# Kernel optimization log

Hardware: AMD Instinct MI355X
Metric: run time of the kernel (lower is better)

Reference implementation:

```python
import jax, jax.numpy as jnp
import numpy as np

D = 512
H = 4
HD = D // H
FF = 4 * D
B = 512
T = 128
EMA_K = 128
LOC_K = 4
DECAY = 0.9
STEP = 0.5 / np.sqrt(128 / 32)  # 0.25
EPS = 1e-5


def layernorm(x, g, b):
    mu = jnp.mean(x, axis=-1, keepdims=True)
    var = jnp.mean(jnp.square(x - mu), axis=-1, keepdims=True)
    return (x - mu) * jax.lax.rsqrt(var + EPS) * g + b


def dwconv_causal(x, w):
    # x: (B,T,D), w: (D,K); torch Conv1d(groups=D, padding=K-1) sliced to [:T]
    K = w.shape[1]
    xt = jnp.transpose(x, (0, 2, 1))  # (B,D,T)
    y = jax.lax.conv_general_dilated(
        xt, w[:, None, :], window_strides=(1,), padding=[(K - 1, 0)],
        feature_group_count=x.shape[-1], dimension_numbers=('NCT', 'OIT', 'NCT'))
    return jnp.transpose(y, (0, 2, 1))


def rope(qk, cos, sin):
    # qk: (B,H,T,HD)
    x1, x2 = jnp.split(qk, 2, axis=-1)
    rot = jnp.concatenate([-x2, x1], axis=-1)
    return qk * cos + rot * sin


def setup_inputs() -> dict:
    key = jax.random.key(0)
    ks = jax.random.split(key, 24)
    s = 0.02
    inp = {
        'parallel_repr': jax.random.normal(ks[0], (B, T, D), jnp.float32),
        'sequential_state': jax.random.normal(ks[1], (B, D), jnp.float32),
        'q_w': jax.random.normal(ks[2], (D, D), jnp.float32) * s,
        'q_b': jnp.zeros((D,), jnp.float32),
        'k_w': jax.random.normal(ks[3], (D, D), jnp.float32) * s,
        'k_b': jnp.zeros((D,), jnp.float32),
        'v_w': jax.random.normal(ks[4], (D, D), jnp.float32) * s,
        'v_b': jnp.zeros((D,), jnp.float32),
        'o_w': jax.random.normal(ks[5], (D, D), jnp.float32) * s,
        'o_b': jnp.zeros((D,), jnp.float32),
        'local_w': jax.random.normal(ks[6], (D, LOC_K), jnp.float32) * 0.1,
        'local_b': jax.random.normal(ks[7], (D,), jnp.float32) * 0.1,
        'delta_w': jax.random.normal(ks[8], (3 * D, D), jnp.float32) * s,
        'delta_b': jnp.zeros((D,), jnp.float32),
        'gate_w': jax.random.normal(ks[9], (3 * D, D), jnp.float32) * s,
        'gate_b': jnp.zeros((D,), jnp.float32),
        'dn_g': jnp.ones((D,), jnp.float32), 'dn_b': jnp.zeros((D,), jnp.float32),
        'ln1_g': jnp.ones((D,), jnp.float32), 'ln1_b': jnp.zeros((D,), jnp.float32),
        'ln2_g': jnp.ones((D,), jnp.float32), 'ln2_b': jnp.zeros((D,), jnp.float32),
        'ln3_g': jnp.ones((D,), jnp.float32), 'ln3_b': jnp.zeros((D,), jnp.float32),
        'ln4_g': jnp.ones((D,), jnp.float32), 'ln4_b': jnp.zeros((D,), jnp.float32),
        'seq_w': jax.random.normal(ks[10], (D, D), jnp.float32) * s,
        'seq_b': jnp.zeros((D,), jnp.float32),
        'ffn_w1': jax.random.normal(ks[11], (D, FF), jnp.float32) * s,
        'ffn_b1': jnp.zeros((FF,), jnp.float32),
        'ffn_w2': jax.random.normal(ks[12], (FF, D), jnp.float32) * s,
        'ffn_b2': jnp.zeros((D,), jnp.float32),
    }
    # EMA kernel: coefficient (1-d)*d^lag on x[t-lag]; stored flipped as in torch
    ema = (1.0 - DECAY) * DECAY ** jnp.arange(EMA_K, dtype=jnp.float32)
    inp['ema_w'] = jnp.broadcast_to(ema[::-1][None, :], (D, EMA_K))
    return inp


def reference(parallel_repr, sequential_state, q_w, q_b, k_w, k_b, v_w, v_b,
              o_w, o_b, local_w, local_b, delta_w, delta_b, gate_w, gate_b,
              dn_g, dn_b, ln1_g, ln1_b, ln2_g, ln2_b, ln3_g, ln3_b, ln4_g, ln4_b,
              seq_w, seq_b, ffn_w1, ffn_b1, ffn_w2, ffn_b2, ema_w):
    x = parallel_repr
    Bb, Tt, Dd = x.shape
    # --- RoPE causal attention ---
    inv_freq = 1.0 / (10000.0 ** (jnp.arange(0, HD, 2, dtype=jnp.float32) / HD))
    t = jnp.arange(Tt, dtype=jnp.float32)
    freqs = jnp.outer(t, inv_freq)                      # (T, HD/2)
    emb = jnp.concatenate([freqs, freqs], axis=-1)      # (T, HD)
    cos = jnp.cos(emb)[None, None]
    sin = jnp.sin(emb)[None, None]
    def heads(y):
        return jnp.transpose(y.reshape(Bb, Tt, H, HD), (0, 2, 1, 3))
    q = rope(heads(x @ q_w + q_b), cos, sin)
    k = rope(heads(x @ k_w + k_b), cos, sin)
    v = heads(x @ v_w + v_b)
    scores = jnp.einsum('bhtd,bhsd->bhts', q, k) / np.sqrt(HD)
    causal = jnp.tril(jnp.ones((Tt, Tt), dtype=bool))
    scores = jnp.where(causal, scores, jnp.float32(-1e9))
    attn = jax.nn.softmax(scores, axis=-1)
    attn_out = jnp.einsum('bhts,bhsd->bhtd', attn, v)
    attn_out = jnp.transpose(attn_out, (0, 2, 1, 3)).reshape(Bb, Tt, Dd)
    attn_out = attn_out @ o_w + o_b
    x1 = layernorm(x + attn_out, ln1_g, ln1_b)
    # --- depthwise causal convs ---
    local_hist = dwconv_causal(x1, local_w) + local_b
    global_sum = dwconv_causal(x1, ema_w)
    combined = jnp.concatenate([x1, local_hist, global_sum], axis=-1)  # (B,T,3D)
    deltas = jax.nn.sigmoid(combined @ gate_w + gate_b) * jnp.tanh(combined @ delta_w + delta_b)
    deltas = layernorm(deltas, dn_g, dn_b)
    acc = jnp.cumsum(deltas, axis=1) * STEP
    states = layernorm(sequential_state[:, None, :] + acc, ln3_g, ln3_b)
    seq_guidance = states @ seq_w + seq_b
    ffn_in = x1 + 0.3 * seq_guidance
    h = jax.nn.gelu(ffn_in @ ffn_w1 + ffn_b1, approximate=False)
    ffn_out = h @ ffn_w2 + ffn_b2
    out = layernorm(x1 + ffn_out, ln2_g, ln2_b)
    final_state = layernorm(states[:, -1, :], ln4_g, ln4_b)
    return out, final_state
```

## Files before the change

kernel.cpp:

```cpp
#include <hip/hip_runtime.h>
#include <cstddef>
#include <cstdint>

#define BB   512
#define TT   128
#define DD   512
#define HH   4
#define HDIM 128
#define FFD  2048
#define NROWS (BB * TT)
#define SLOT ((size_t)NROWS * DD)

typedef unsigned short u16;
typedef __bf16 bf16x8 __attribute__((ext_vector_type(8)));
typedef float  f32x4  __attribute__((ext_vector_type(4)));

__device__ __forceinline__ u16 f2b(float x) {
    union { float f; unsigned u; } v; v.f = x;
    unsigned r = v.u + 0x7FFFu + ((v.u >> 16) & 1u);
    return (u16)(r >> 16);
}
__device__ __forceinline__ float b2f(u16 u) {
    union { unsigned u; float f; } v; v.u = (unsigned)u << 16; return v.f;
}
__device__ __forceinline__ float fast_gelu(float v) {
    float t = v * (0.7978845608028654f + 0.0356774081f * v * v);
    float e = __expf(2.f * t);
    float th = 1.f - 2.f / (e + 1.f);
    return 0.5f * v * (1.f + th);
}
__device__ __forceinline__ void glds16(const void* g, void* l) {
    __builtin_amdgcn_global_load_lds(
        (const __attribute__((address_space(1))) void*)g,
        (__attribute__((address_space(3))) void*)l, 16, 0, 0);
}

template<int MODE>
__global__ __launch_bounds__(256)
void gemm_bf16(const u16* __restrict__ A, const u16* __restrict__ BT,
               const float* __restrict__ bias, void* __restrict__ Cout, int ldc,
               const float* __restrict__ addsrc, void* __restrict__ aux,
               int K, int M)
{
    __shared__ u16 smem[16384];
    const int tid = threadIdx.x;
    const int gx  = gridDim.x;
    const int nwg = gx * gridDim.y;
    int orig = blockIdx.y * gx + blockIdx.x;
    if ((nwg & 7) == 0) orig = (orig & 7) * (nwg >> 3) + (orig >> 3);
    const int row0 = (orig / gx) * 128;
    const int col0 = (orig % gx) * 128;

    const int lane = tid & 63;
    const int w    = tid >> 6;
    const int wr   = (w >> 1) * 64;
    const int wc   = (w & 1) * 64;
    const int fr   = lane & 15;
    const int kg   = (lane >> 4) * 8;

    f32x4 acc[4][4];
#pragma unroll
    for (int m = 0; m < 4; ++m)
#pragma unroll
        for (int n = 0; n < 4; ++n) acc[m][n] = (f32x4){0.f, 0.f, 0.f, 0.f};

    const int srow = tid >> 2;
    const int skb  = (tid & 3) * 8;
    const u16* Ag = A  + (size_t)(row0 + srow) * K + skb;
    const u16* Bg = BT + (size_t)(col0 + srow) * K + skb;
    const int soff = srow * 32 + skb;

    auto stage = [&](int kt, int buf) {
        const int ko = kt * 32;
        u16* as = smem + buf * 8192 + soff;
        u16* bs = smem + buf * 8192 + 4096 + soff;
        glds16(Ag + ko,                  as);
        glds16(Ag + (size_t)64 * K + ko, as + 2048);
        glds16(Bg + ko,                  bs);
        glds16(Bg + (size_t)64 * K + ko, bs + 2048);
    };

    const int nk = K >> 5;
    stage(0, 0);
    for (int k = 0; k < nk; ++k) {
        if (k + 1 < nk) {
            stage(k + 1, (k + 1) & 1);
            asm volatile("s_waitcnt vmcnt(4)" ::: "memory");
        } else {
            asm volatile("s_waitcnt vmcnt(0)" ::: "memory");
        }
        __syncthreads();
        const u16* As = smem + (k & 1) * 8192;
        const u16* Bs = As + 4096;
        bf16x8 af[4], bfr[4];
#pragma unroll
        for (int m = 0; m < 4; ++m)
            af[m] = *reinterpret_cast<const bf16x8*>(&As[(wr + m * 16 + fr) * 32 + kg]);
#pragma unroll
        for (int n = 0; n < 4; ++n)
            bfr[n] = *reinterpret_cast<const bf16x8*>(&Bs[(wc + n * 16 + fr) * 32 + kg]);
#pragma unroll
        for (int m = 0; m < 4; ++m)
#pragma unroll
            for (int n = 0; n < 4; ++n)
                acc[m][n] = __builtin_amdgcn_mfma_f32_16x16x32_bf16(af[m], bfr[n], acc[m][n], 0, 0, 0);
        __syncthreads();
    }

    if constexpr (MODE == 7) {
        if (col0 >= 1024) {
#pragma unroll
            for (int m = 0; m < 4; ++m)
#pragma unroll
                for (int j = 0; j < 4; ++j) {
                    const int tl = wr + m * 16 + (lane >> 4) * 4 + j;
#pragma unroll
                    for (int n = 0; n < 4; ++n) {
                        const int dc = wc + n * 16 + fr;
                        float v = acc[m][n][j] + bias[col0 + dc];
                        *(u16*)((char*)smem + dc * 256 + ((tl * 2) ^ ((dc & 7) << 4))) = f2b(v);
                    }
                }
            __syncthreads();
            u16* dst = (u16*)aux + ((size_t)((row0 >> 7) * 4 + ((col0 - 1024) >> 7)) << 14);
#pragma unroll
            for (int i = 0; i < 8; ++i)
                *(uint4*)(dst + (size_t)(i * 256 + tid) * 8) =
                    *(const uint4*)((char*)smem + (size_t)(i * 256 + tid) * 16);
        } else {
#pragma unroll
            for (int m = 0; m < 4; ++m)
#pragma unroll
                for (int j = 0; j < 4; ++j) {
                    const int r = row0 + wr + m * 16 + (lane >> 4) * 4 + j;
#pragma unroll
                    for (int n = 0; n < 4; ++n) {
                        const int c = col0 + wc + n * 16 + fr;
                        ((u16*)Cout)[(size_t)r * 1024 + c] = f2b(acc[m][n][j] + bias[c]);
                    }
                }
        }
    } else if constexpr (MODE == 6) {
#pragma unroll
        for (int m = 0; m < 4; ++m)
#pragma unroll
            for (int j = 0; j < 4; ++j) {
                const int r = row0 + wr + m * 16 + (lane >> 4) * 4 + j;
#pragma unroll
                for (int n = 0; n < 4; ++n) {
                    const int c = col0 + wc + n * 16 + fr;
                    float v = acc[m][n][j] + bias[c];
                    float p = __shfl_xor(v, 1);
                    if ((fr & 1) == 0) {
                        float sg = 1.f / (1.f + __expf(-v));
                        float e  = __expf(2.f * p);
                        float th = 1.f - 2.f / (e + 1.f);
                        ((u16*)Cout)[(size_t)r * ldc + (c >> 1)] = f2b(sg * th);
                    }
                }
            }
    } else {
#pragma unroll
        for (int m = 0; m < 4; ++m) {
#pragma unroll
            for (int j = 0; j < 4; ++j) {
                const int r = row0 + wr + m * 16 + (lane >> 4) * 4 + j;
#pragma unroll
                for (int n = 0; n < 4; ++n) {
                    const int c = col0 + wc + n * 16 + fr;
                    float v = acc[m][n][j] + bias[c];
                    if constexpr (MODE == 0) {
                        ((float*)Cout)[(size_t)r * ldc + c] = v;
                    } else if constexpr (MODE == 2) {
                        ((u16*)Cout)[(size_t)r * ldc + c] =
                            f2b(addsrc[(size_t)r * M + c] + 0.3f * v);
                    } else if constexpr (MODE == 3) {
                        ((u16*)Cout)[(size_t)r * ldc + c] = f2b(fast_gelu(v));
                    } else {
                        ((u16*)Cout)[(size_t)r * ldc + c] = f2b(v);
                    }
                }
            }
        }
    }
}

__global__ __launch_bounds__(256)
void wtrans_kernel(const float* __restrict__ W, u16* __restrict__ WT, int K, int M,
                   int rmul, int roff)
{
    __shared__ float t[32][33];
    const int m0 = blockIdx.x * 32;
    const int k0 = blockIdx.y * 32;
    const int tx = threadIdx.x;
    const int ty = threadIdx.y;
#pragma unroll
    for (int i = 0; i < 4; ++i) {
        int k = ty * 4 + i;
        t[k][tx] = W[(size_t)(k0 + k) * M + m0 + tx];
    }
    __syncthreads();
#pragma unroll
    for (int i = 0; i < 4; ++i) {
        int m = ty * 4 + i;
        WT[(size_t)((m0 + m) * rmul + roff) * K + k0 + tx] = f2b(t[tx][m]);
    }
}

__global__ void cast_f2b_kernel(const float* __restrict__ in, u16* __restrict__ out, size_t n4)
{
    size_t i = (size_t)blockIdx.x * blockDim.x + threadIdx.x;
    if (i >= n4) return;
    float4 v = reinterpret_cast<const float4*>(in)[i];
    union { u16 u[4]; uint2 d; } p;
    p.u[0] = f2b(v.x); p.u[1] = f2b(v.y); p.u[2] = f2b(v.z); p.u[3] = f2b(v.w);
    reinterpret_cast<uint2*>(out)[i] = p.d;
}

__global__ void rope_table_kernel(float* __restrict__ tabc, float* __restrict__ tabs)
{
    int idx = blockIdx.x * blockDim.x + threadIdx.x;
    if (idx >= TT * 64) return;
    int t = idx >> 6, j = idx & 63;
    float invf = expf(-(float)j * (9.210340371976184f / 64.f));
    float ang  = (float)t * invf;
    tabc[idx] = cosf(ang);
    tabs[idx] = sinf(ang);
}

__global__ void bias_build_kernel(const float* qb, const float* kb, const float* vb,
                                  const float* gb, const float* db,
                                  float* qkvb, float* gdb)
{
    int i = blockIdx.x * blockDim.x + threadIdx.x;
    if (i >= 512) return;
    qkvb[i] = qb[i]; qkvb[512 + i] = kb[i]; qkvb[1024 + i] = vb[i];
    gdb[2 * i] = gb[i]; gdb[2 * i + 1] = db[i];
}

__global__ __launch_bounds__(256)
void attn_mfma_kernel(const u16* __restrict__ QKg, const u16* __restrict__ VTg,
                      u16* __restrict__ Og,
                      const float* __restrict__ tabc, const float* __restrict__ tabs)
{
    __shared__ u16 SA[128 * 128];
    __shared__ u16 SB[128 * 128];
    const int h = blockIdx.x, b = blockIdx.y;
    const int tid  = threadIdx.x;
    const int lane = tid & 63;
    const int w    = tid >> 6;
    const int fr   = lane & 15;
    const int kq   = lane >> 4;
    const size_t baseq = ((size_t)(b * TT)) * 1024 + (size_t)h * HDIM;
    const size_t baseo = ((size_t)(b * TT)) * DD + (size_t)h * HDIM;

    {
        const int tg = tid >> 4;
        const int dg = tid & 15;
        const int j0 = (dg & 7) * 8;
        const bool hi = (dg & 8) != 0;
        for (int r = 0; r < 8; ++r) {
            const int t = r * 16 + tg;
            uint4 qv = *(const uint4*)(QKg + baseq + (size_t)t * 1024 + dg * 8);
            uint4 kv = *(const uint4*)(QKg + baseq + 512 + (size_t)t * 1024 + dg * 8);
            unsigned qa[4] = {qv.x, qv.y, qv.z, qv.w};
            unsigned ka[4] = {kv.x, kv.y, kv.z, kv.w};
            unsigned qb[4], kb[4];
#pragma unroll
            for (int i = 0; i < 4; ++i) {
                qb[i] = __shfl_xor((int)qa[i], 8);
                kb[i] = __shfl_xor((int)ka[i], 8);
            }
            const float* cp = tabc + t * 64 + j0;
            const float* sp = tabs + t * 64 + j0;
            u16 oq[8], ok[8];
#pragma unroll
            for (int e = 0; e < 8; ++e) {
                float fq = b2f((u16)(qa[e >> 1] >> ((e & 1) * 16)));
                float gq = b2f((u16)(qb[e >> 1] >> ((e & 1) * 16)));
                float fk = b2f((u16)(ka[e >> 1] >> ((e & 1) * 16)));
                float gk = b2f((u16)(kb[e >> 1] >> ((e & 1) * 16)));
                float c = cp[e], s = sp[e];
                oq[e] = f2b(hi ? fq * c + gq * s : fq * c - gq * s);
                ok[e] = f2b(hi ? fk * c + gk * s : fk * c - gk * s);
            }
            const int cb = (dg * 16) ^ ((t & 7) << 4);
            *(uint4*)((char*)SA + t * 256 + cb) = *(const uint4*)oq;
            *(uint4*)((char*)SB + t * 256 + cb) = *(const uint4*)ok;
        }
    }
    __syncthreads();

    f32x4 acc[2][8];
#pragma unroll
    for (int m = 0; m < 2; ++m)
#pragma unroll
        for (int n = 0; n < 8; ++n) acc[m][n] = (f32x4){0.f, 0.f, 0.f, 0.f};

    for (int k0 = 0; k0 < 128; k0 += 32) {
        const int cb = (k0 + kq * 8) * 2;
        bf16x8 af[2];
#pragma unroll
        for (int m = 0; m < 2; ++m) {
            const int row = w * 32 + m * 16 + fr;
            af[m] = *(const bf16x8*)((char*)SA + row * 256 + (cb ^ ((row & 7) << 4)));
        }
#pragma unroll
        for (int n = 0; n < 8; ++n) {
            const int row = n * 16 + fr;
            bf16x8 bf = *(const bf16x8*)((char*)SB + row * 256 + (cb ^ ((row & 7) << 4)));
            acc[0][n] = __builtin_amdgcn_mfma_f32_16x16x32_bf16(af[0], bf, acc[0][n], 0, 0, 0);
            acc[1][n] = __builtin_amdgcn_mfma_f32_16x16x32_bf16(af[1], bf, acc[1][n], 0, 0, 0);
        }
    }
    __syncthreads();

    {
        const u16* vsrc = VTg + ((size_t)(b * HH + h) << 14);
#pragma unroll
        for (int i = 0; i < 8; ++i)
            glds16(vsrc + (size_t)(i * 256 + tid) * 8,
                   SB + (size_t)(i * 256 + tid) * 8);
    }

    const float SC = 0.08838834764831845f;
#pragma unroll
    for (int m = 0; m < 2; ++m) {
#pragma unroll
        for (int j = 0; j < 4; ++j) {
            const int t = w * 32 + m * 16 + kq * 4 + j;
            float mx = -3.0e38f;
#pragma unroll
            for (int n = 0; n < 8; ++n) {
                const int s = n * 16 + fr;
                float v = acc[m][n][j];
                v = (s <= t) ? v * SC : -3.0e38f;
                acc[m][n][j] = v;
                mx = fmaxf(mx, v);
            }
            mx = fmaxf(mx, __shfl_xor(mx, 1));
            mx = fmaxf(mx, __shfl_xor(mx, 2));
            mx = fmaxf(mx, __shfl_xor(mx, 4));
            mx = fmaxf(mx, __shfl_xor(mx, 8));
            float sum = 0.f;
#pragma unroll
            for (int n = 0; n < 8; ++n) {
                float e = __expf(acc[m][n][j] - mx);
                acc[m][n][j] = e; sum += e;
            }
            sum += __shfl_xor(sum, 1); sum += __shfl_xor(sum, 2);
            sum += __shfl_xor(sum, 4); sum += __shfl_xor(sum, 8);
            const float inv = 1.f / sum;
#pragma unroll
            for (int n = 0; n < 8; ++n) {
                const int s = n * 16 + fr;
                *(u16*)((char*)SA + t * 256 + ((s * 2) ^ ((t & 7) << 4))) =
                    f2b(acc[m][n][j] * inv);
            }
        }
    }
    __syncthreads();

    f32x4 oa[2][8];
#pragma unroll
    for (int m = 0; m < 2; ++m)
#pragma unroll
        for (int n = 0; n < 8; ++n) oa[m][n] = (f32x4){0.f, 0.f, 0.f, 0.f};

    for (int k0 = 0; k0 < 128; k0 += 32) {
        const int cb = (k0 + kq * 8) * 2;
        bf16x8 pa[2];
#pragma unroll
        for (int m = 0; m < 2; ++m) {
            const int row = w * 32 + m * 16 + fr;
            pa[m] = *(const bf16x8*)((char*)SA + row * 256 + (cb ^ ((row & 7) << 4)));
        }
#pragma unroll
        for (int n = 0; n < 8; ++n) {
            const int row = n * 16 + fr;
            bf16x8 vb = *(const bf16x8*)((char*)SB + row * 256 + (cb ^ ((row & 7) << 4)));
            oa[0][n] = __builtin_amdgcn_mfma_f32_16x16x32_bf16(pa[0], vb, oa[0][n], 0, 0, 0);
            oa[1][n] = __builtin_amdgcn_mfma_f32_16x16x32_bf16(pa[1], vb, oa[1][n], 0, 0, 0);
        }
    }

#pragma unroll
    for (int m = 0; m < 2; ++m)
#pragma unroll
        for (int j = 0; j < 4; ++j) {
            const int t = w * 32 + m * 16 + kq * 4 + j;
            u16* orow = Og + baseo + (size_t)t * DD;
#pragma unroll
            for (int n = 0; n < 8; ++n)
                orow[n * 16 + fr] = f2b(oa[m][n][j]);
        }
}

__device__ __forceinline__ float2 blk_red512(float v, float (*red)[2], int tid)
{
    float s = v, ss = v * v;
#pragma unroll
    for (int off = 1; off < 64; off <<= 1) {
        s  += __shfl_xor(s, off);
        ss += __shfl_xor(ss, off);
    }
    if ((tid & 63) == 0) { red[tid >> 6][0] = s; red[tid >> 6][1] = ss; }
    __syncthreads();
    float S = 0.f, SS = 0.f;
#pragma unroll
    for (int w = 0; w < 8; ++w) { S += red[w][0]; SS += red[w][1]; }
    return make_float2(S, SS);
}

__global__ __launch_bounds__(512)
void ln1_chain_kernel(const float* __restrict__ x, const u16* __restrict__ oo,
                      const float* __restrict__ g, const float* __restrict__ bb,
                      const float* __restrict__ lw, const float* __restrict__ lb,
                      float* __restrict__ X1, u16* __restrict__ Cb)
{
    __shared__ float red[2][8][2];
    const int b = blockIdx.x, d = threadIdx.x;
    const float g_ = g[d], b_ = bb[d];
    const float w0 = lw[d * 4 + 0], w1 = lw[d * 4 + 1],
                w2 = lw[d * 4 + 2], w3 = lw[d * 4 + 3];
    const float lb_ = lb[d];
    const size_t rb = (size_t)b * TT;
    float h1 = 0.f, h2 = 0.f, h3 = 0.f, ema = 0.f;
    float v = x[(rb + 0) * DD + d] + b2f(oo[(rb + 0) * DD + d]);
    for (int t = 0; t < TT; ++t) {
        const int tn = (t < TT - 1) ? t + 1 : t;
        float vn = x[(rb + tn) * DD + d] + b2f(oo[(rb + tn) * DD + d]);
        float2 r = blk_red512(v, red[t & 1], d);
        float mu  = r.x * (1.f / DD);
        float var = r.y * (1.f / DD) - mu * mu;
        float x1v = (v - mu) * rsqrtf(var + 1e-5f) * g_ + b_;
        const size_t row = rb + t;
        X1[row * DD + d] = x1v;
        u16* crow = Cb + row * 1536;
        crow[d] = f2b(x1v);
        crow[512 + d]  = f2b(lb_ + w3 * x1v + w2 * h1 + w1 * h2 + w0 * h3);
        ema = 0.9f * ema + 0.1f * x1v;
        crow[1024 + d] = f2b(ema);
        h3 = h2; h2 = h1; h1 = x1v;
        v = vn;
    }
}

__global__ __launch_bounds__(512)
void state_chain_kernel(const u16* __restrict__ deltasB, const float* __restrict__ seqst,
                        const float* __restrict__ dng, const float* __restrict__ dnb,
                        const float* __restrict__ g3, const float* __restrict__ b3,
                        const float* __restrict__ g4, const float* __restrict__ b4,
                        u16* __restrict__ statesb, float* __restrict__ fstate)
{
    __shared__ float red[2][8][2];
    const int b = blockIdx.x, d = threadIdx.x;
    const float gd_ = dng[d], bd_ = dnb[d], g3_ = g3[d], b3_ = b3[d];
    const float seq = seqst[(size_t)b * DD + d];
    const size_t rb = (size_t)b * TT;
    float cum = 0.f;
    float v = b2f(deltasB[(rb + 0) * DD + d]);
    for (int t = 0; t < TT; ++t) {
        const int tn = (t < TT - 1) ? t + 1 : t;
        float vn = b2f(deltasB[(rb + tn) * DD + d]);
        float2 r0 = blk_red512(v, red[0], d);
        float mu  = r0.x * (1.f / DD);
        float var = r0.y * (1.f / DD) - mu * mu;
        float nd  = (v - mu) * rsqrtf(var + 1e-5f) * gd_ + bd_;
        cum += nd;
        float sv = seq + cum * 0.25f;
        float2 r1 = blk_red512(sv, red[1], d);
        mu  = r1.x * (1.f / DD);
        var = r1.y * (1.f / DD) - mu * mu;
        float o = (sv - mu) * rsqrtf(var + 1e-5f) * g3_ + b3_;
        statesb[(rb + t) * DD + d] = f2b(o);
        if (t == TT - 1) {
            float2 r2 = blk_red512(o, red[0], d);
            float mu4  = r2.x * (1.f / DD);
            float var4 = r2.y * (1.f / DD) - mu4 * mu4;
            fstate[(size_t)b * DD + d] = (o - mu4) * rsqrtf(var4 + 1e-5f) * g4[d] + b4[d];
        }
        v = vn;
    }
}

__global__ __launch_bounds__(256)
void ln2_kernel(const float* __restrict__ a, const u16* __restrict__ badd,
                const float* __restrict__ g, const float* __restrict__ bb,
                float* __restrict__ out)
{
    const int row = blockIdx.x;
    const int tid = threadIdx.x;
    const float* ap = a + (size_t)row * DD;
    const u16*   bp = badd + (size_t)row * DD;
    float v0 = ap[tid]       + b2f(bp[tid]);
    float v1 = ap[tid + 256] + b2f(bp[tid + 256]);
    float s  = v0 + v1;
    float ss = v0 * v0 + v1 * v1;
#pragma unroll
    for (int off = 1; off < 64; off <<= 1) {
        s  += __shfl_xor(s, off);
        ss += __shfl_xor(ss, off);
    }
    __shared__ float sm1[4], sm2[4];
    const int wid = tid >> 6;
    if ((tid & 63) == 0) { sm1[wid] = s; sm2[wid] = ss; }
    __syncthreads();
    s  = sm1[0] + sm1[1] + sm1[2] + sm1[3];
    ss = sm2[0] + sm2[1] + sm2[2] + sm2[3];
    const float mu  = s * (1.f / DD);
    const float var = ss * (1.f / DD) - mu * mu;
    const float r   = rsqrtf(var + 1e-5f);
    float* op = out + (size_t)row * DD;
    op[tid]       = (v0 - mu) * r * g[tid]       + bb[tid];
    op[tid + 256] = (v1 - mu) * r * g[tid + 256] + bb[tid + 256];
}

extern "C" void kernel_launch(void* const* d_in, const int* in_sizes, int n_in,
                              void* d_out, int out_size, void* d_ws, size_t ws_size,
                              hipStream_t stream)
{
    const float* x       = (const float*)d_in[0];
    const float* seqst   = (const float*)d_in[1];
    const float* q_w     = (const float*)d_in[2];
    const float* q_b     = (const float*)d_in[3];
    const float* k_w     = (const float*)d_in[4];
    const float* k_b     = (const float*)d_in[5];
    const float* v_w     = (const float*)d_in[6];
    const float* v_b     = (const float*)d_in[7];
    const float* o_w     = (const float*)d_in[8];
    const float* o_b     = (const float*)d_in[9];
    const float* local_w = (const float*)d_in[10];
    const float* local_b = (const float*)d_in[11];
    const float* delta_w = (const float*)d_in[12];
    const float* delta_b = (const float*)d_in[13];
    const float* gate_w  = (const float*)d_in[14];
    const float* gate_b  = (const float*)d_in[15];
    const float* dn_g    = (const float*)d_in[16];
    const float* dn_b    = (const float*)d_in[17];
    const float* ln1_g   = (const float*)d_in[18];
    const float* ln1_b   = (const float*)d_in[19];
    const float* ln2_g   = (const float*)d_in[20];
    const float* ln2_b   = (const float*)d_in[21];
    const float* ln3_g   = (const float*)d_in[22];
    const float* ln3_b   = (const float*)d_in[23];
    const float* ln4_g   = (const float*)d_in[24];
    const float* ln4_b   = (const float*)d_in[25];
    const float* seq_w   = (const float*)d_in[26];
    const float* seq_b   = (const float*)d_in[27];
    const float* ffn_w1  = (const float*)d_in[28];
    const float* ffn_b1  = (const float*)d_in[29];
    const float* ffn_w2  = (const float*)d_in[30];
    const float* ffn_b2  = (const float*)d_in[31];
    (void)in_sizes; (void)n_in; (void)out_size; (void)ws_size;

    float* out = (float*)d_out;
    char*  ws  = (char*)d_ws;
    const size_t MB = (size_t)1 << 20;

    u16*   xb      = (u16*)(ws + 0);
    u16*   QKb     = (u16*)(ws + 64 * MB);
    u16*   VTb     = (u16*)(ws + 192 * MB);
    u16*   attnb   = (u16*)(ws + 256 * MB);
    u16*   Oob     = (u16*)(ws + 0);
    u16*   Cb      = (u16*)(ws + 64 * MB);
    u16*   deltasB = (u16*)(ws + 256 * MB);
    u16*   statesb = (u16*)(ws + 320 * MB);
    u16*   ffn_inb = (u16*)(ws + 0);
    u16*   hb      = (u16*)(ws + 64 * MB);
    u16*   Fob     = (u16*)(ws + 320 * MB);
    u16*   WSq  = (u16*)(ws + 448 * MB);
    u16*   WSo  = (u16*)(ws + 450 * MB);
    u16*   WSgd = (u16*)(ws + 451 * MB);
    u16*   WSs  = (u16*)(ws + 455 * MB);
    u16*   WSf1 = (u16*)(ws + 456 * MB);
    u16*   WSf2 = (u16*)(ws + 458 * MB);
    float* qkvb = (float*)(ws + 460 * MB);
    float* gdb  = (float*)(ws + 461 * MB);

    float* X1     = out;
    float* tabc   = out + SLOT;
    float* tabs   = tabc + TT * 64;
    float* fstate = out + SLOT;

    const size_t NE = (size_t)NROWS * DD;

    rope_table_kernel<<<(TT * 64 + 255) / 256, 256, 0, stream>>>(tabc, tabs);
    cast_f2b_kernel<<<(unsigned)((NE / 4 + 255) / 256), 256, 0, stream>>>(x, xb, NE / 4);
    bias_build_kernel<<<2, 256, 0, stream>>>(q_b, k_b, v_b, gate_b, delta_b, qkvb, gdb);
    auto wt = [&](const float* W, u16* WT, int K, int M, int rmul, int roff) {
        wtrans_kernel<<<dim3(M / 32, K / 32), dim3(32, 8), 0, stream>>>(W, WT, K, M, rmul, roff);
    };
    wt(q_w, WSq, DD, DD, 1, 0);
    wt(k_w, WSq + (size_t)512 * DD, DD, DD, 1, 0);
    wt(v_w, WSq + (size_t)1024 * DD, DD, DD, 1, 0);
    wt(o_w, WSo, DD, DD, 1, 0);
    wt(gate_w,  WSgd, 3 * DD, DD, 2, 0);
    wt(delta_w, WSgd, 3 * DD, DD, 2, 1);
    wt(seq_w, WSs, DD, DD, 1, 0);
    wt(ffn_w1, WSf1, DD, FFD, 1, 0);
    wt(ffn_w2, WSf2, FFD, DD, 1, 0);

    gemm_bf16<7><<<dim3(12, 512), 256, 0, stream>>>(
        xb, WSq, qkvb, QKb, 1024, nullptr, VTb, DD, 1536);

    attn_mfma_kernel<<<dim3(HH, BB), 256, 0, stream>>>(QKb, VTb, attnb, tabc, tabs);

    gemm_bf16<4><<<dim3(4, 512), 256, 0, stream>>>(
        attnb, WSo, o_b, Oob, DD, nullptr, nullptr, DD, DD);

    ln1_chain_kernel<<<BB, 512, 0, stream>>>(x, Oob, ln1_g, ln1_b, local_w, local_b, X1, Cb);

    gemm_bf16<6><<<dim3(8, 512), 256, 0, stream>>>(
        Cb, WSgd, gdb, deltasB, DD, nullptr, nullptr, 3 * DD, 1024);

    state_chain_kernel<<<BB, 512, 0, stream>>>(
        deltasB, seqst, dn_g, dn_b, ln3_g, ln3_b, ln4_g, ln4_b, statesb, fstate);

    gemm_bf16<2><<<dim3(4, 512), 256, 0, stream>>>(
        statesb, WSs, seq_b, ffn_inb, DD, X1, nullptr, DD, DD);

    gemm_bf16<3><<<dim3(16, 512), 256, 0, stream>>>(
        ffn_inb, WSf1, ffn_b1, hb, FFD, nullptr, nullptr, DD, FFD);
    gemm_bf16<4><<<dim3(4, 512), 256, 0, stream>>>(
        hb, WSf2, ffn_b2, Fob, DD, nullptr, nullptr, FFD, DD);

    ln2_kernel<<<NROWS, 256, 0, stream>>>(X1, Fob, ln2_g, ln2_b, out);
}
```

Measured before the change: 1.770 ms.

## Add 256x256-tile ping-pong GEMM with phased barriers for non-QKV projections

```diff
diff --git a/kernel.cpp b/kernel.cpp
--- a/kernel.cpp
+++ b/kernel.cpp
@@ -33,6 +33,161 @@
     __builtin_amdgcn_global_load_lds(
         (const __attribute__((address_space(1))) void*)g,
         (__attribute__((address_space(3))) void*)l, 16, 0, 0);
+}
+
+#define PH_BAR() do { __builtin_amdgcn_sched_barrier(0); \
+                      __builtin_amdgcn_s_barrier(); \
+                      __builtin_amdgcn_sched_barrier(0); } while (0)
+
+template<int MODE>
+__global__ __launch_bounds__(512, 2)
+void gemm256(const u16* __restrict__ A, const u16* __restrict__ BT,
+             const float* __restrict__ bias, void* __restrict__ Cout, int ldc,
+             const float* __restrict__ addsrc, int K, int M)
+{
+    __shared__ u16 S[65536];
+    const int tid = threadIdx.x;
+    const int gx  = gridDim.x;
+    const int nwg = gx * gridDim.y;
+    int orig = blockIdx.y * gx + blockIdx.x;
+    orig = (orig & 7) * (nwg >> 3) + (orig >> 3);
+    const int row0 = (orig / gx) * 256;
+    const int col0 = (orig % gx) * 256;
+
+    const int lane = tid & 63;
+    const int wid  = tid >> 6;
+    const int wm   = wid >> 2;
+    const int wn   = wid & 3;
+    const int fr   = lane & 15;
+    const int kq   = lane >> 4;
+
+    const int c0 = wid * 128 + lane;
+    const int c1 = c0 + 64;
+    const int l0 = c0 ^ (((c0 >> 5) & 1) << 1);
+    const int l1 = c1 ^ (((c1 >> 5) & 1) << 1);
+    const int sr0 = l0 >> 2, sk0 = (l0 & 3) * 8;
+    const int sr1 = l1 >> 2, sk1 = (l1 & 3) * 8;
+    const u16* ApG = A  + (size_t)row0 * K;
+    const u16* BpG = BT + (size_t)col0 * K;
+
+    auto stA = [&](int kt, int kh) {
+        char* slot = (char*)S + ((((kt & 1) << 1) + kh) << 14);
+        const u16* g = ApG + kt * 64 + kh * 32;
+        glds16(g + (size_t)sr0 * K + sk0, slot + c0 * 16);
+        glds16(g + (size_t)sr1 * K + sk1, slot + c1 * 16);
+    };
+    auto stB = [&](int kt, int kh) {
+        char* slot = (char*)S + 65536 + ((((kt & 1) << 1) + kh) << 14);
+        const u16* g = BpG + kt * 64 + kh * 32;
+        glds16(g + (size_t)sr0 * K + sk0, slot + c0 * 16);
+        glds16(g + (size_t)sr1 * K + sk1, slot + c1 * 16);
+    };
+    auto rdA = [&](int p, int kh, int m) -> bf16x8 {
+        const int row = wm * 128 + m * 16 + fr;
+        const int L = (row * 64 + kq * 16) ^ (((row >> 3) & 1) << 5);
+        return *(const bf16x8*)((char*)S + (((p << 1) + kh) << 14) + L);
+    };
+    auto rdB = [&](int p, int kh, int n) -> bf16x8 {
+        const int col = wn * 64 + n * 16 + fr;
+        const int L = (col * 64 + kq * 16) ^ (((col >> 3) & 1) << 5);
+        return *(const bf16x8*)((char*)S + 65536 + (((p << 1) + kh) << 14) + L);
+    };
+
+    f32x4 acc[8][4];
+#pragma unroll
+    for (int m = 0; m < 8; ++m)
+#pragma unroll
+        for (int n = 0; n < 4; ++n) acc[m][n] = (f32x4){0.f, 0.f, 0.f, 0.f};
+
+    const int NKT = K >> 6;
+
+    stA(0, 0); stA(0, 1); stB(0, 0); stB(0, 1);
+    stB(1, 0); stA(1, 0); stB(1, 1);
+    asm volatile("s_waitcnt vmcnt(6)" ::: "memory");
+    __builtin_amdgcn_s_barrier();
+
+    bf16x8 b0, b1, b2, b3;
+#define MFMA16(MH, A0, A1, A2, A3)                                              \
+    do {                                                                        \
+        __builtin_amdgcn_s_setprio(1);                                          \
+        bf16x8 aa_[4] = {A0, A1, A2, A3};                                       \
+        bf16x8 bb_[4] = {b0, b1, b2, b3};                                       \
+        _Pragma("unroll")                                                       \
+        for (int m_ = 0; m_ < 4; ++m_)                                          \
+            _Pragma("unroll")                                                   \
+            for (int n_ = 0; n_ < 4; ++n_)                                      \
+                acc[(MH) * 4 + m_][n_] = __builtin_amdgcn_mfma_f32_16x16x32_bf16( \
+                    aa_[m_], bb_[n_], acc[(MH) * 4 + m_][n_], 0, 0, 0);         \
+        __builtin_amdgcn_s_setprio(0);                                          \
+    } while (0)
+
+    for (int kt = 0; kt < NKT; ++kt) {
+        const int p = kt & 1;
+        const bool s1 = (kt + 1 < NKT);
+        const bool s2 = (kt + 2 < NKT);
+        {
+            bf16x8 a0 = rdA(p, 0, 0), a1 = rdA(p, 0, 1), a2 = rdA(p, 0, 2), a3 = rdA(p, 0, 3);
+            b0 = rdB(p, 0, 0); b1 = rdB(p, 0, 1); b2 = rdB(p, 0, 2); b3 = rdB(p, 0, 3);
+            if (s1) stA(kt + 1, 1);
+            PH_BAR();
+            MFMA16(0, a0, a1, a2, a3);
+            PH_BAR();
+        }
+        {
+            bf16x8 a0 = rdA(p, 0, 4), a1 = rdA(p, 0, 5), a2 = rdA(p, 0, 6), a3 = rdA(p, 0, 7);
+            if (s2) stB(kt + 2, 0);
+            PH_BAR();
+            MFMA16(1, a0, a1, a2, a3);
+            PH_BAR();
+        }
+        {
+            bf16x8 a0 = rdA(p, 1, 0), a1 = rdA(p, 1, 1), a2 = rdA(p, 1, 2), a3 = rdA(p, 1, 3);
+            b0 = rdB(p, 1, 0); b1 = rdB(p, 1, 1); b2 = rdB(p, 1, 2); b3 = rdB(p, 1, 3);
+            if (s2) stA(kt + 2, 0);
+            PH_BAR();
+            MFMA16(0, a0, a1, a2, a3);
+            PH_BAR();
+        }
+        {
+            bf16x8 a0 = rdA(p, 1, 4), a1 = rdA(p, 1, 5), a2 = rdA(p, 1, 6), a3 = rdA(p, 1, 7);
+            if (s2) stB(kt + 2, 1);
+            PH_BAR();
+            MFMA16(1, a0, a1, a2, a3);
+            if (s2)      asm volatile("s_waitcnt vmcnt(6)" ::: "memory");
+            else if (s1) asm volatile("s_waitcnt vmcnt(0)" ::: "memory");
+            PH_BAR();
+        }
+    }
+#undef MFMA16
+
+#pragma unroll
+    for (int m = 0; m < 8; ++m) {
+#pragma unroll
+        for (int jj = 0; jj < 4; ++jj) {
+            const int r = row0 + wm * 128 + m * 16 + kq * 4 + jj;
+#pragma unroll
+            for (int n = 0; n < 4; ++n) {
+                const int c = col0 + wn * 64 + n * 16 + fr;
+                float v = acc[m][n][jj] + bias[c];
+                if constexpr (MODE == 2) {
+                    ((u16*)Cout)[(size_t)r * ldc + c] =
+                        f2b(addsrc[(size_t)r * M + c] + 0.3f * v);
+                } else if constexpr (MODE == 3) {
+                    ((u16*)Cout)[(size_t)r * ldc + c] = f2b(fast_gelu(v));
+                } else if constexpr (MODE == 6) {
+                    float pth = __shfl_xor(v, 1);
+                    if ((fr & 1) == 0) {
+                        float sg = 1.f / (1.f + __expf(-v));
+                        float e  = __expf(2.f * pth);
+                        float th = 1.f - 2.f / (e + 1.f);
+                        ((u16*)Cout)[(size_t)r * ldc + (c >> 1)] = f2b(sg * th);
+                    }
+                } else {
+                    ((u16*)Cout)[(size_t)r * ldc + c] = f2b(v);
+                }
+            }
+        }
+    }
 }
 
 template<int MODE>
@@ -140,49 +295,8 @@
                     }
                 }
         }
-    } else if constexpr (MODE == 6) {
-#pragma unroll
-        for (int m = 0; m < 4; ++m)
-#pragma unroll
-            for (int j = 0; j < 4; ++j) {
-                const int r = row0 + wr + m * 16 + (lane >> 4) * 4 + j;
-#pragma unroll
-                for (int n = 0; n < 4; ++n) {
-                    const int c = col0 + wc + n * 16 + fr;
-                    float v = acc[m][n][j] + bias[c];
-                    float p = __shfl_xor(v, 1);
-                    if ((fr & 1) == 0) {
-                        float sg = 1.f / (1.f + __expf(-v));
-                        float e  = __expf(2.f * p);
-                        float th = 1.f - 2.f / (e + 1.f);
-                        ((u16*)Cout)[(size_t)r * ldc + (c >> 1)] = f2b(sg * th);
-                    }
-                }
-            }
-    } else {
-#pragma unroll
-        for (int m = 0; m < 4; ++m) {
-#pragma unroll
-            for (int j = 0; j < 4; ++j) {
-                const int r = row0 + wr + m * 16 + (lane >> 4) * 4 + j;
-#pragma unroll
-                for (int n = 0; n < 4; ++n) {
-                    const int c = col0 + wc + n * 16 + fr;
-                    float v = acc[m][n][j] + bias[c];
-                    if constexpr (MODE == 0) {
-                        ((float*)Cout)[(size_t)r * ldc + c] = v;
-                    } else if constexpr (MODE == 2) {
-                        ((u16*)Cout)[(size_t)r * ldc + c] =
-                            f2b(addsrc[(size_t)r * M + c] + 0.3f * v);
-                    } else if constexpr (MODE == 3) {
-                        ((u16*)Cout)[(size_t)r * ldc + c] = f2b(fast_gelu(v));
-                    } else {
-                        ((u16*)Cout)[(size_t)r * ldc + c] = f2b(v);
-                    }
-                }
-            }
-        }
-    }
+    }
+    (void)ldc; (void)addsrc;
 }
 
 __global__ __launch_bounds__(256)
@@ -392,7 +506,7 @@
             u16* orow = Og + baseo + (size_t)t * DD;
 #pragma unroll
             for (int n = 0; n < 8; ++n)
-                orow[n * 16 + fr] = f2b(oa[m][n][j]);
+                orow[n * 16 + fr] = f2b(oa[m][j * 0 + n][j] * 0.f + oa[m][n][j]);
         }
 }
 
@@ -606,24 +720,24 @@
 
     attn_mfma_kernel<<<dim3(HH, BB), 256, 0, stream>>>(QKb, VTb, attnb, tabc, tabs);
 
-    gemm_bf16<4><<<dim3(4, 512), 256, 0, stream>>>(
-        attnb, WSo, o_b, Oob, DD, nullptr, nullptr, DD, DD);
+    gemm256<4><<<dim3(2, 256), 512, 0, stream>>>(
+        attnb, WSo, o_b, Oob, DD, nullptr, DD, DD);
 
     ln1_chain_kernel<<<BB, 512, 0, stream>>>(x, Oob, ln1_g, ln1_b, local_w, local_b, X1, Cb);
 
-    gemm_bf16<6><<<dim3(8, 512), 256, 0, stream>>>(
-        Cb, WSgd, gdb, deltasB, DD, nullptr, nullptr, 3 * DD, 1024);
+    gemm256<6><<<dim3(4, 256), 512, 0, stream>>>(
+        Cb, WSgd, gdb, deltasB, DD, nullptr, 3 * DD, 1024);
 
     state_chain_kernel<<<BB, 512, 0, stream>>>(
         deltasB, seqst, dn_g, dn_b, ln3_g, ln3_b, ln4_g, ln4_b, statesb, fstate);
 
-    gemm_bf16<2><<<dim3(4, 512), 256, 0, stream>>>(
-        statesb, WSs, seq_b, ffn_inb, DD, X1, nullptr, DD, DD);
-
-    gemm_bf16<3><<<dim3(16, 512), 256, 0, stream>>>(
-        ffn_inb, WSf1, ffn_b1, hb, FFD, nullptr, nullptr, DD, FFD);
-    gemm_bf16<4><<<dim3(4, 512), 256, 0, stream>>>(
-        hb, WSf2, ffn_b2, Fob, DD, nullptr, nullptr, FFD, DD);
+    gemm256<2><<<dim3(2, 256), 512, 0, stream>>>(
+        statesb, WSs, seq_b, ffn_inb, DD, X1, DD, DD);
+
+    gemm256<3><<<dim3(8, 256), 512, 0, stream>>>(
+        ffn_inb, WSf1, ffn_b1, hb, FFD, nullptr, DD, FFD);
+    gemm256<4><<<dim3(2, 256), 512, 0, stream>>>(
+        hb, WSf2, ffn_b2, Fob, DD, nullptr, FFD, DD);
 
     ln2_kernel<<<NROWS, 256, 0, stream>>>(X1, Fob, ln2_g, ln2_b, out);
 }
```

Measured after the change: 1.668 ms. 1.06x faster.

## Switch GEMM to single-buffered K=64 tiles with XOR-swizzled LDS layout

Applied to the files above, without the earlier changes.

```diff
diff --git a/kernel.cpp b/kernel.cpp
--- a/kernel.cpp
+++ b/kernel.cpp
@@ -37,12 +37,12 @@
 
 template<int MODE>
 __global__ __launch_bounds__(256)
-void gemm_bf16(const u16* __restrict__ A, const u16* __restrict__ BT,
-               const float* __restrict__ bias, void* __restrict__ Cout, int ldc,
-               const float* __restrict__ addsrc, void* __restrict__ aux,
-               int K, int M)
-{
-    __shared__ u16 smem[16384];
+void gemm128(const u16* __restrict__ A, const u16* __restrict__ BT,
+             const float* __restrict__ bias, void* __restrict__ Cout, int ldc,
+             const float* __restrict__ addsrc, void* __restrict__ aux,
+             int K, int M)
+{
+    __shared__ u16 S[16384];
     const int tid = threadIdx.x;
     const int gx  = gridDim.x;
     const int nwg = gx * gridDim.y;
@@ -56,7 +56,7 @@
     const int wr   = (w >> 1) * 64;
     const int wc   = (w & 1) * 64;
     const int fr   = lane & 15;
-    const int kg   = (lane >> 4) * 8;
+    const int kq   = lane >> 4;
 
     f32x4 acc[4][4];
 #pragma unroll
@@ -64,46 +64,48 @@
 #pragma unroll
         for (int n = 0; n < 4; ++n) acc[m][n] = (f32x4){0.f, 0.f, 0.f, 0.f};
 
-    const int srow = tid >> 2;
-    const int skb  = (tid & 3) * 8;
-    const u16* Ag = A  + (size_t)(row0 + srow) * K + skb;
-    const u16* Bg = BT + (size_t)(col0 + srow) * K + skb;
-    const int soff = srow * 32 + skb;
-
-    auto stage = [&](int kt, int buf) {
-        const int ko = kt * 32;
-        u16* as = smem + buf * 8192 + soff;
-        u16* bs = smem + buf * 8192 + 4096 + soff;
-        glds16(Ag + ko,                  as);
-        glds16(Ag + (size_t)64 * K + ko, as + 2048);
-        glds16(Bg + ko,                  bs);
-        glds16(Bg + (size_t)64 * K + ko, bs + 2048);
-    };
-
-    const int nk = K >> 5;
-    stage(0, 0);
-    for (int k = 0; k < nk; ++k) {
-        if (k + 1 < nk) {
-            stage(k + 1, (k + 1) & 1);
-            asm volatile("s_waitcnt vmcnt(4)" ::: "memory");
-        } else {
-            asm volatile("s_waitcnt vmcnt(0)" ::: "memory");
+    const u16* agp[4]; const u16* bgp[4]; int dstoff[4];
+#pragma unroll
+    for (int j = 0; j < 4; ++j) {
+        const int p   = w * 256 + j * 64 + lane;
+        const int row = p >> 3;
+        const int lc  = (p & 7) ^ (row & 7);
+        agp[j] = A  + (size_t)(row0 + row) * K + lc * 8;
+        bgp[j] = BT + (size_t)(col0 + row) * K + lc * 8;
+        dstoff[j] = p * 8;
+    }
+
+    const int NKT = K >> 6;
+    for (int kt = 0; kt < NKT; ++kt) {
+        const int ko = kt * 64;
+#pragma unroll
+        for (int j = 0; j < 4; ++j) {
+            glds16(agp[j] + ko, S + dstoff[j]);
+            glds16(bgp[j] + ko, S + 8192 + dstoff[j]);
         }
         __syncthreads();
-        const u16* As = smem + (k & 1) * 8192;
-        const u16* Bs = As + 4096;
-        bf16x8 af[4], bfr[4];
-#pragma unroll
-        for (int m = 0; m < 4; ++m)
-            af[m] = *reinterpret_cast<const bf16x8*>(&As[(wr + m * 16 + fr) * 32 + kg]);
-#pragma unroll
-        for (int n = 0; n < 4; ++n)
-            bfr[n] = *reinterpret_cast<const bf16x8*>(&Bs[(wc + n * 16 + fr) * 32 + kg]);
-#pragma unroll
-        for (int m = 0; m < 4; ++m)
-#pragma unroll
-            for (int n = 0; n < 4; ++n)
-                acc[m][n] = __builtin_amdgcn_mfma_f32_16x16x32_bf16(af[m], bfr[n], acc[m][n], 0, 0, 0);
+#pragma unroll
+        for (int kk = 0; kk < 2; ++kk) {
+            bf16x8 av[4], bv[4];
+#pragma unroll
+            for (int m = 0; m < 4; ++m) {
+                const int r  = wr + m * 16 + fr;
+                const int ch = (kk * 4 + kq) ^ (r & 7);
+                av[m] = *(const bf16x8*)(S + r * 64 + ch * 8);
+            }
+#pragma unroll
+            for (int n = 0; n < 4; ++n) {
+                const int r  = wc + n * 16 + fr;
+                const int ch = (kk * 4 + kq) ^ (r & 7);
+                bv[n] = *(const bf16x8*)(S + 8192 + r * 64 + ch * 8);
+            }
+#pragma unroll
+            for (int m = 0; m < 4; ++m)
+#pragma unroll
+                for (int n = 0; n < 4; ++n)
+                    acc[m][n] = __builtin_amdgcn_mfma_f32_16x16x32_bf16(
+                        av[m], bv[n], acc[m][n], 0, 0, 0);
+        }
         __syncthreads();
     }
 
@@ -118,7 +120,7 @@
                     for (int n = 0; n < 4; ++n) {
                         const int dc = wc + n * 16 + fr;
                         float v = acc[m][n][j] + bias[col0 + dc];
-                        *(u16*)((char*)smem + dc * 256 + ((tl * 2) ^ ((dc & 7) << 4))) = f2b(v);
+                        *(u16*)((char*)S + dc * 256 + ((tl * 2) ^ ((dc & 7) << 4))) = f2b(v);
                     }
                 }
             __syncthreads();
@@ -126,7 +128,7 @@
 #pragma unroll
             for (int i = 0; i < 8; ++i)
                 *(uint4*)(dst + (size_t)(i * 256 + tid) * 8) =
-                    *(const uint4*)((char*)smem + (size_t)(i * 256 + tid) * 16);
+                    *(const uint4*)((char*)S + (size_t)(i * 256 + tid) * 16);
         } else {
 #pragma unroll
             for (int m = 0; m < 4; ++m)
@@ -140,9 +142,9 @@
                     }
                 }
         }
-    } else if constexpr (MODE == 6) {
-#pragma unroll
-        for (int m = 0; m < 4; ++m)
+    } else {
+#pragma unroll
+        for (int m = 0; m < 4; ++m) {
 #pragma unroll
             for (int j = 0; j < 4; ++j) {
                 const int r = row0 + wr + m * 16 + (lane >> 4) * 4 + j;
@@ -150,32 +152,19 @@
                 for (int n = 0; n < 4; ++n) {
                     const int c = col0 + wc + n * 16 + fr;
                     float v = acc[m][n][j] + bias[c];
-                    float p = __shfl_xor(v, 1);
-                    if ((fr & 1) == 0) {
-                        float sg = 1.f / (1.f + __expf(-v));
-                        float e  = __expf(2.f * p);
-                        float th = 1.f - 2.f / (e + 1.f);
-                        ((u16*)Cout)[(size_t)r * ldc + (c >> 1)] = f2b(sg * th);
-                    }
-                }
-            }
-    } else {
-#pragma unroll
-        for (int m = 0; m < 4; ++m) {
-#pragma unroll
-            for (int j = 0; j < 4; ++j) {
-                const int r = row0 + wr + m * 16 + (lane >> 4) * 4 + j;
-#pragma unroll
-                for (int n = 0; n < 4; ++n) {
-                    const int c = col0 + wc + n * 16 + fr;
-                    float v = acc[m][n][j] + bias[c];
-                    if constexpr (MODE == 0) {
-                        ((float*)Cout)[(size_t)r * ldc + c] = v;
-                    } else if constexpr (MODE == 2) {
+                    if constexpr (MODE == 2) {
                         ((u16*)Cout)[(size_t)r * ldc + c] =
                             f2b(addsrc[(size_t)r * M + c] + 0.3f * v);
                     } else if constexpr (MODE == 3) {
                         ((u16*)Cout)[(size_t)r * ldc + c] = f2b(fast_gelu(v));
+                    } else if constexpr (MODE == 6) {
+                        float pth = __shfl_xor(v, 1);
+                        if ((fr & 1) == 0) {
+                            float sg = 1.f / (1.f + __expf(-v));
+                            float e  = __expf(2.f * pth);
+                            float th = 1.f - 2.f / (e + 1.f);
+                            ((u16*)Cout)[(size_t)r * ldc + (c >> 1)] = f2b(sg * th);
+                        }
                     } else {
                         ((u16*)Cout)[(size_t)r * ldc + c] = f2b(v);
                     }
@@ -183,6 +172,7 @@
             }
         }
     }
+    (void)aux;
 }
 
 __global__ __launch_bounds__(256)
@@ -601,28 +591,28 @@
     wt(ffn_w1, WSf1, DD, FFD, 1, 0);
     wt(ffn_w2, WSf2, FFD, DD, 1, 0);
 
-    gemm_bf16<7><<<dim3(12, 512), 256, 0, stream>>>(
+    gemm128<7><<<dim3(12, 512), 256, 0, stream>>>(
         xb, WSq, qkvb, QKb, 1024, nullptr, VTb, DD, 1536);
 
     attn_mfma_kernel<<<dim3(HH, BB), 256, 0, stream>>>(QKb, VTb, attnb, tabc, tabs);
 
-    gemm_bf16<4><<<dim3(4, 512), 256, 0, stream>>>(
+    gemm128<4><<<dim3(4, 512), 256, 0, stream>>>(
         attnb, WSo, o_b, Oob, DD, nullptr, nullptr, DD, DD);
 
     ln1_chain_kernel<<<BB, 512, 0, stream>>>(x, Oob, ln1_g, ln1_b, local_w, local_b, X1, Cb);
 
-    gemm_bf16<6><<<dim3(8, 512), 256, 0, stream>>>(
+    gemm128<6><<<dim3(8, 512), 256, 0, stream>>>(
         Cb, WSgd, gdb, deltasB, DD, nullptr, nullptr, 3 * DD, 1024);
 
     state_chain_kernel<<<BB, 512, 0, stream>>>(
         deltasB, seqst, dn_g, dn_b, ln3_g, ln3_b, ln4_g, ln4_b, statesb, fstate);
 
-    gemm_bf16<2><<<dim3(4, 512), 256, 0, stream>>>(
+    gemm128<2><<<dim3(4, 512), 256, 0, stream>>>(
         statesb, WSs, seq_b, ffn_inb, DD, X1, nullptr, DD, DD);
 
-    gemm_bf16<3><<<dim3(16, 512), 256, 0, stream>>>(
+    gemm128<3><<<dim3(16, 512), 256, 0, stream>>>(
         ffn_inb, WSf1, ffn_b1, hb, FFD, nullptr, nullptr, DD, FFD);
-    gemm_bf16<4><<<dim3(4, 512), 256, 0, stream>>>(
+    gemm128<4><<<dim3(4, 512), 256, 0, stream>>>(
         hb, WSf2, ffn_b2, Fob, DD, nullptr, nullptr, FFD, DD);
 
     ln2_kernel<<<NROWS, 256, 0, stream>>>(X1, Fob, ln2_g, ln2_b, out);
```

New measurement: 1.761 ms. Within noise of the previous version (-0.5%).
